# Performance work log

Hardware: AMD Instinct MI355X
Metric: run time of the kernel (lower is better)

## Reference

```python
import jax, jax.numpy as jnp
import numpy as np

IN_SIZE = 256
N_THETA = 180
GRID = int(np.ceil(np.sqrt(2.0) * IN_SIZE))  # 363, == detector size == it_size


def _ramp_filter(P):
    # f is the spatial-domain ramp filter impulse response (Ram-Lak)
    n = np.concatenate([np.arange(1, P / 2 + 1, 2), np.arange(P / 2 - 1, 0, -2)])
    f = np.zeros(P, np.float32)
    f[0] = 0.25
    f[1::2] = -1.0 / (np.pi * n) ** 2
    # torch code multiplies both re/im by the real part of fft(f): complex * real scalar
    return jnp.asarray(2.0 * np.real(np.fft.fft(f)), jnp.float32)  # [P]


def _apply_ramp(x):
    # x: [N,C,S,A]; FFT filter along detector axis (2) with zero padding
    S = x.shape[2]
    P = max(64, int(2 ** np.ceil(np.log2(2 * S))))
    xp = jnp.pad(x, ((0, 0), (0, 0), (0, P - S), (0, 0)))
    filt = _ramp_filter(P)  # [P]
    spec = jnp.fft.fft(xp, axis=2) * filt[:, None]
    return jnp.real(jnp.fft.ifft(spec, axis=2))[:, :, :S, :].astype(x.dtype)


def _polar_T(G):
    # T[a,i,j] = xgrid*cos(theta_a) - ygrid*sin(theta_a), grids via meshgrid(ij)
    unit = jnp.linspace(-1.0, 1.0, G, dtype=jnp.float32)
    yg, xg = jnp.meshgrid(unit, unit, indexing='ij')
    th = jnp.deg2rad(jnp.arange(N_THETA, dtype=jnp.float32))  # [A]
    return xg[None] * jnp.cos(th)[:, None, None] - yg[None] * jnp.sin(th)[:, None, None]  # [A,G,G]


def _backproject(sino, T):
    # sino: [N,C,S,A]; grid X coord = i*2/(A-1)-1 picks column a exactly
    # (align_corners=True), so bilinear reduces to 1D lerp along the detector.
    N, C, S, A = sino.shape
    G = T.shape[1]
    pos = (T + 1.0) * (S - 1) / 2.0  # [A,G,G] fractional detector index
    i0 = jnp.floor(pos)
    w = (pos - i0).reshape(A, -1)  # [A,G*G]
    i0i = i0.astype(jnp.int32)
    i1i = i0i + 1
    ok0 = ((i0i >= 0) & (i0i < S)).reshape(A, -1)  # zeros padding outside
    ok1 = ((i1i >= 0) & (i1i < S)).reshape(A, -1)
    i0c = jnp.clip(i0i, 0, S - 1).reshape(A, -1)
    i1c = jnp.clip(i1i, 0, S - 1).reshape(A, -1)
    st = jnp.moveaxis(sino, 3, 2)  # [N,C,A,S]
    v0 = jnp.take_along_axis(st, i0c[None, None], axis=3)  # [N,C,A,G*G]
    v1 = jnp.take_along_axis(st, i1c[None, None], axis=3)
    w0 = jnp.where(ok0, 1.0 - w, 0.0)[None, None]
    w1 = jnp.where(ok1, w, 0.0)[None, None]
    reco = (v0 * w0 + v1 * w1).sum(axis=2)  # sum over angles
    return reco.reshape(N, C, G, G)


def setup_inputs() -> dict:
    key = jax.random.key(0)
    x = jax.random.normal(key, (4, 1, GRID, N_THETA), dtype=jnp.float32)
    return {"x": x}


def reference(x) -> jnp.ndarray:
    # filtered backprojection (inverse Radon), circle=False
    x = _apply_ramp(x)
    T = _polar_T(GRID)
    reco = _backproject(x, T)  # [N,C,G,G]
    # crop back to in_size x in_size (negative padding in torch code)
    W, G = IN_SIZE, GRID
    pad = G - W
    pad_before = (W + pad) // 2 - W // 2
    reco = reco[:, :, pad_before:G - (pad - pad_before), pad_before:G - (pad - pad_before)]
    return reco * (jnp.pi / (2.0 * N_THETA))
```

## Files before the change

kernel.cpp:

```cpp
#include <hip/hip_runtime.h>

#define S_DIM 363
#define S_P   368
#define A_DIM 180
#define OUT_W 256
#define F_PI 3.14159265358979323846f

typedef float    f4 __attribute__((ext_vector_type(4)));
typedef _Float16 h4 __attribute__((ext_vector_type(4)));
union HU { uint2 u; h4 h; };

__device__ uint2 g_sino[A_DIM * S_P];

__global__ __launch_bounds__(192) void iradon_filter_kernel(
        const float* __restrict__ x) {
    __shared__ f4    xs4[S_DIM];
    __shared__ float wt[192];

    const int a   = blockIdx.x;
    const int tid = threadIdx.x;

    {
        f4 v;
        v.x = x[(0 * S_DIM + tid) * A_DIM + a];
        v.y = x[(1 * S_DIM + tid) * A_DIM + a];
        v.z = x[(2 * S_DIM + tid) * A_DIM + a];
        v.w = x[(3 * S_DIM + tid) * A_DIM + a];
        xs4[tid] = v;
        const int s2 = tid + 192;
        if (s2 < S_DIM) {
            f4 w;
            w.x = x[(0 * S_DIM + s2) * A_DIM + a];
            w.y = x[(1 * S_DIM + s2) * A_DIM + a];
            w.z = x[(2 * S_DIM + s2) * A_DIM + a];
            w.w = x[(3 * S_DIM + s2) * A_DIM + a];
            xs4[s2] = w;
        }
    }
    {
        float d = (float)(2 * tid + 1);
        wt[tid] = -2.0f / (F_PI * F_PI * d * d);
    }
    __syncthreads();

    const int t1 = tid;
    const int t2 = tid + 192;
    f4 acc1 = 0.5f * xs4[t1];
    f4 acc2 = 0.5f * xs4[(t2 < S_DIM) ? t2 : 0];

    const int s0 = 1 - (tid & 1);
    #pragma unroll 4
    for (int s = s0; s < S_DIM; s += 2) {
        f4 v = xs4[s];
        int d1 = s - t1; d1 = (d1 < 0) ? -d1 : d1;
        int d2 = s - t2; d2 = (d2 < 0) ? -d2 : d2;
        acc1 += wt[d1 >> 1] * v;
        acc2 += wt[d2 >> 1] * v;
    }

    HU r1; r1.h = __builtin_convertvector(acc1, h4);
    g_sino[a * S_P + 1 + t1] = r1.u;
    if (t2 < S_DIM) {
        HU r2; r2.h = __builtin_convertvector(acc2, h4);
        g_sino[a * S_P + 1 + t2] = r2.u;
    }
    if (tid == 190) { HU z; z.u.x = 0u; z.u.y = 0u; g_sino[a * S_P + 0]   = z.u; }
    if (tid == 191) { HU z; z.u.x = 0u; z.u.y = 0u; g_sino[a * S_P + 364] = z.u; }
}

__global__ __launch_bounds__(256) void iradon_backproject_kernel(
        float* __restrict__ out) {
    __shared__ float2 csn[A_DIM];
    __shared__ f4 red[256];

    const int tid = threadIdx.x;
    if (tid < A_DIM) {
        float th = (float)tid * (F_PI / 180.0f);
        csn[tid] = make_float2(cosf(th), sinf(th));
    }
    __syncthreads();

    const int px = tid & 63;
    const int q  = tid >> 6;
    const int j  = blockIdx.x * 64 + px;
    const int i  = blockIdx.y;

    const float jj  = (float)(j - 128);
    const float nii = (float)(128 - i);

    f4 acc = (f4)0.0f;
    const int a0 = q * 45;
    #pragma unroll 5
    for (int m = 0; m < 45; ++m) {
        const int a = a0 + m;
        const float2 cn = csn[a];
        float pos = fmaf(jj, cn.x, fmaf(nii, cn.y, 181.0f));
        float f   = floorf(pos);
        int   k1  = (int)f + 1;
        float w1  = pos - f;
        float w0  = 1.0f - w1;
        const uint2* __restrict__ row = g_sino + a * S_P;
        HU lo, hi;
        lo.u = row[k1];
        hi.u = row[k1 + 1];
        acc.x = fmaf((float)lo.h.x, w0, fmaf((float)hi.h.x, w1, acc.x));
        acc.y = fmaf((float)lo.h.y, w0, fmaf((float)hi.h.y, w1, acc.y));
        acc.z = fmaf((float)lo.h.z, w0, fmaf((float)hi.h.z, w1, acc.z));
        acc.w = fmaf((float)lo.h.w, w0, fmaf((float)hi.h.w, w1, acc.w));
    }

    red[tid] = acc;
    __syncthreads();

    if (tid < 64) {
        f4 r = red[tid] + red[tid + 64] + red[tid + 128] + red[tid + 192];
        r *= (F_PI / 360.0f);
        const int jo   = blockIdx.x * 64 + tid;
        const size_t p = (size_t)blockIdx.y * OUT_W + jo;
        out[p]              = r.x;
        out[p +     65536]  = r.y;
        out[p + 2 * 65536]  = r.z;
        out[p + 3 * 65536]  = r.w;
    }
}

extern "C" void kernel_launch(void* const* d_in, const int* in_sizes, int n_in,
                              void* d_out, int out_size, void* d_ws, size_t ws_size,
                              hipStream_t stream) {
    const float* x = (const float*)d_in[0];
    float* out = (float*)d_out;

    iradon_filter_kernel<<<dim3(A_DIM), 192, 0, stream>>>(x);
    iradon_backproject_kernel<<<dim3(4, OUT_W), 256, 0, stream>>>(out);
}
```

Measured before the change: 73.70 us.

## Fuse filter and backprojection into one persistent kernel with grid barrier

Merges the ramp-filter kernel and the backprojection kernel into a single launch of 512 blocks. The first 180 blocks filter one angle each, then every block waits at a software grid-wide barrier built on an atomic counter, and afterwards each block backprojects two output rows. This removes one kernel launch and the inter-kernel gap, in exchange for barrier spin cost and a reliance on all 512 blocks being co-resident, which deadlocks if they are not. Each block now does twice the backprojection work, so there is less parallelism per block.

```diff
diff --git a/kernel.cpp b/kernel.cpp
--- a/kernel.cpp
+++ b/kernel.cpp
@@ -4,6 +4,7 @@
 #define S_P   368
 #define A_DIM 180
 #define OUT_W 256
+#define GRIDN 512
 #define F_PI 3.14159265358979323846f
 
 typedef float    f4 __attribute__((ext_vector_type(4)));
@@ -12,115 +13,135 @@
 
 __device__ uint2 g_sino[A_DIM * S_P];
 
-__global__ __launch_bounds__(192) void iradon_filter_kernel(
-        const float* __restrict__ x) {
-    __shared__ f4    xs4[S_DIM];
-    __shared__ float wt[192];
+__device__ unsigned g_bar = 0u;
 
-    const int a   = blockIdx.x;
-    const int tid = threadIdx.x;
-
-    {
-        f4 v;
-        v.x = x[(0 * S_DIM + tid) * A_DIM + a];
-        v.y = x[(1 * S_DIM + tid) * A_DIM + a];
-        v.z = x[(2 * S_DIM + tid) * A_DIM + a];
-        v.w = x[(3 * S_DIM + tid) * A_DIM + a];
-        xs4[tid] = v;
-        const int s2 = tid + 192;
-        if (s2 < S_DIM) {
-            f4 w;
-            w.x = x[(0 * S_DIM + s2) * A_DIM + a];
-            w.y = x[(1 * S_DIM + s2) * A_DIM + a];
-            w.z = x[(2 * S_DIM + s2) * A_DIM + a];
-            w.w = x[(3 * S_DIM + s2) * A_DIM + a];
-            xs4[s2] = w;
-        }
-    }
-    {
-        float d = (float)(2 * tid + 1);
-        wt[tid] = -2.0f / (F_PI * F_PI * d * d);
-    }
-    __syncthreads();
-
-    const int t1 = tid;
-    const int t2 = tid + 192;
-    f4 acc1 = 0.5f * xs4[t1];
-    f4 acc2 = 0.5f * xs4[(t2 < S_DIM) ? t2 : 0];
-
-    const int s0 = 1 - (tid & 1);
-    #pragma unroll 4
-    for (int s = s0; s < S_DIM; s += 2) {
-        f4 v = xs4[s];
-        int d1 = s - t1; d1 = (d1 < 0) ? -d1 : d1;
-        int d2 = s - t2; d2 = (d2 < 0) ? -d2 : d2;
-        acc1 += wt[d1 >> 1] * v;
-        acc2 += wt[d2 >> 1] * v;
-    }
-
-    HU r1; r1.h = __builtin_convertvector(acc1, h4);
-    g_sino[a * S_P + 1 + t1] = r1.u;
-    if (t2 < S_DIM) {
-        HU r2; r2.h = __builtin_convertvector(acc2, h4);
-        g_sino[a * S_P + 1 + t2] = r2.u;
-    }
-    if (tid == 190) { HU z; z.u.x = 0u; z.u.y = 0u; g_sino[a * S_P + 0]   = z.u; }
-    if (tid == 191) { HU z; z.u.x = 0u; z.u.y = 0u; g_sino[a * S_P + 364] = z.u; }
-}
-
-__global__ __launch_bounds__(256) void iradon_backproject_kernel(
-        float* __restrict__ out) {
+__global__ __launch_bounds__(256, 2) void iradon_fused_kernel(
+        const float* __restrict__ x, float* __restrict__ out) {
+    __shared__ f4     xs4[S_DIM];
+    __shared__ float  wt[256];
     __shared__ float2 csn[A_DIM];
-    __shared__ f4 red[256];
+    __shared__ f4     red[256];
 
     const int tid = threadIdx.x;
+    const int b   = blockIdx.x;
+
     if (tid < A_DIM) {
         float th = (float)tid * (F_PI / 180.0f);
         csn[tid] = make_float2(cosf(th), sinf(th));
+    }
+
+    if (b < A_DIM) {
+        const int a = b;
+        {
+            f4 v;
+            v.x = x[(0 * S_DIM + tid) * A_DIM + a];
+            v.y = x[(1 * S_DIM + tid) * A_DIM + a];
+            v.z = x[(2 * S_DIM + tid) * A_DIM + a];
+            v.w = x[(3 * S_DIM + tid) * A_DIM + a];
+            xs4[tid] = v;
+            const int s2 = tid + 256;
+            if (s2 < S_DIM) {
+                f4 w;
+                w.x = x[(0 * S_DIM + s2) * A_DIM + a];
+                w.y = x[(1 * S_DIM + s2) * A_DIM + a];
+                w.z = x[(2 * S_DIM + s2) * A_DIM + a];
+                w.w = x[(3 * S_DIM + s2) * A_DIM + a];
+                xs4[s2] = w;
+            }
+        }
+        {
+            float d = (float)(2 * tid + 1);
+            wt[tid] = -2.0f / (F_PI * F_PI * d * d);
+        }
+        __syncthreads();
+
+        if (tid < 192) {
+            const int t1 = tid;
+            const int t2 = tid + 192;
+            f4 acc1 = 0.5f * xs4[t1];
+            f4 acc2 = 0.5f * xs4[(t2 < S_DIM) ? t2 : 0];
+
+            const int s0 = 1 - (tid & 1);
+            #pragma unroll 4
+            for (int s = s0; s < S_DIM; s += 2) {
+                f4 v = xs4[s];
+                int d1 = s - t1; d1 = (d1 < 0) ? -d1 : d1;
+                int d2 = s - t2; d2 = (d2 < 0) ? -d2 : d2;
+                acc1 += wt[d1 >> 1] * v;
+                acc2 += wt[d2 >> 1] * v;
+            }
+
+            HU r1; r1.h = __builtin_convertvector(acc1, h4);
+            g_sino[a * S_P + 1 + t1] = r1.u;
+            if (t2 < S_DIM) {
+                HU r2; r2.h = __builtin_convertvector(acc2, h4);
+                g_sino[a * S_P + 1 + t2] = r2.u;
+            }
+        }
+        if (tid == 252) { HU z; z.u.x = 0u; z.u.y = 0u; g_sino[a * S_P + 0]   = z.u; }
+        if (tid == 253) { HU z; z.u.x = 0u; z.u.y = 0u; g_sino[a * S_P + 364] = z.u; }
+    }
+
+    __syncthreads();
+    if (tid == 0) {
+        __threadfence();
+        unsigned t = __hip_atomic_fetch_add(&g_bar, 1u, __ATOMIC_ACQ_REL,
+                                            __HIP_MEMORY_SCOPE_AGENT);
+        unsigned target = (t / GRIDN + 1u) * GRIDN;
+        while (__hip_atomic_load(&g_bar, __ATOMIC_ACQUIRE,
+                                 __HIP_MEMORY_SCOPE_AGENT) < target) {
+            __builtin_amdgcn_s_sleep(2);
+        }
+        __threadfence();
     }
     __syncthreads();
 
     const int px = tid & 63;
     const int q  = tid >> 6;
-    const int j  = blockIdx.x * 64 + px;
-    const int i  = blockIdx.y;
+    const int jx = b & 3;
+    const int j  = jx * 64 + px;
+    const float jj = (float)(j - 128);
+    const int a0 = q * 45;
 
-    const float jj  = (float)(j - 128);
-    const float nii = (float)(128 - i);
+    #pragma unroll 2
+    for (int half = 0; half < 2; ++half) {
+        const int i = (b >> 2) + half * 128;
+        const float nii = (float)(128 - i);
 
-    f4 acc = (f4)0.0f;
-    const int a0 = q * 45;
-    #pragma unroll 5
-    for (int m = 0; m < 45; ++m) {
-        const int a = a0 + m;
-        const float2 cn = csn[a];
-        float pos = fmaf(jj, cn.x, fmaf(nii, cn.y, 181.0f));
-        float f   = floorf(pos);
-        int   k1  = (int)f + 1;
-        float w1  = pos - f;
-        float w0  = 1.0f - w1;
-        const uint2* __restrict__ row = g_sino + a * S_P;
-        HU lo, hi;
-        lo.u = row[k1];
-        hi.u = row[k1 + 1];
-        acc.x = fmaf((float)lo.h.x, w0, fmaf((float)hi.h.x, w1, acc.x));
-        acc.y = fmaf((float)lo.h.y, w0, fmaf((float)hi.h.y, w1, acc.y));
-        acc.z = fmaf((float)lo.h.z, w0, fmaf((float)hi.h.z, w1, acc.z));
-        acc.w = fmaf((float)lo.h.w, w0, fmaf((float)hi.h.w, w1, acc.w));
-    }
+        f4 acc = (f4)0.0f;
+        #pragma unroll 5
+        for (int m = 0; m < 45; ++m) {
+            const int a = a0 + m;
+            const float2 cn = csn[a];
+            float pos = fmaf(jj, cn.x, fmaf(nii, cn.y, 181.0f));
+            float f   = floorf(pos);
+            int   k1  = (int)f + 1;
+            float w1  = pos - f;
+            float w0  = 1.0f - w1;
+            const uint2* __restrict__ row = g_sino + a * S_P;
+            HU lo, hi;
+            lo.u = row[k1];
+            hi.u = row[k1 + 1];
+            acc.x = fmaf((float)lo.h.x, w0, fmaf((float)hi.h.x, w1, acc.x));
+            acc.y = fmaf((float)lo.h.y, w0, fmaf((float)hi.h.y, w1, acc.y));
+            acc.z = fmaf((float)lo.h.z, w0, fmaf((float)hi.h.z, w1, acc.z));
+            acc.w = fmaf((float)lo.h.w, w0, fmaf((float)hi.h.w, w1, acc.w));
+        }
 
-    red[tid] = acc;
-    __syncthreads();
+        red[tid] = acc;
+        __syncthreads();
 
-    if (tid < 64) {
-        f4 r = red[tid] + red[tid + 64] + red[tid + 128] + red[tid + 192];
-        r *= (F_PI / 360.0f);
-        const int jo   = blockIdx.x * 64 + tid;
-        const size_t p = (size_t)blockIdx.y * OUT_W + jo;
-        out[p]              = r.x;
-        out[p +     65536]  = r.y;
-        out[p + 2 * 65536]  = r.z;
-        out[p + 3 * 65536]  = r.w;
+        if (tid < 64) {
+            f4 r = red[tid] + red[tid + 64] + red[tid + 128] + red[tid + 192];
+            r *= (F_PI / 360.0f);
+            const int jo   = jx * 64 + tid;
+            const size_t p = (size_t)i * OUT_W + jo;
+            out[p]              = r.x;
+            out[p +     65536]  = r.y;
+            out[p + 2 * 65536]  = r.z;
+            out[p + 3 * 65536]  = r.w;
+        }
+        __syncthreads();
     }
 }
 
@@ -130,6 +151,5 @@
     const float* x = (const float*)d_in[0];
     float* out = (float*)d_out;
 
-    iradon_filter_kernel<<<dim3(A_DIM), 192, 0, stream>>>(x);
-    iradon_backproject_kernel<<<dim3(4, OUT_W), 256, 0, stream>>>(out);
+    iradon_fused_kernel<<<dim3(GRIDN), 256, 0, stream>>>(x, out);
 }
```

Measured after the change: 148.8 us. 102% more time.
